# Performance work log

Hardware: AMD Instinct MI355X
Metric: run time of the kernel (lower is better)

The kernel has to match this reference:

```python
import jax, jax.numpy as jnp
import numpy as np


def soft_threshold24(w):
    """2:4 soft-threshold along the last dim: in each contiguous group of 4,
    zero the two smallest magnitudes and shrink the two largest by the
    second-smallest magnitude (sign(w) * relu(|w| - t))."""
    M, N = w.shape
    g = w.reshape(M, N // 4, 4)
    a = jnp.abs(g)
    thr = jnp.sort(a, axis=-1)[..., 1:2]  # 2nd-smallest magnitude per group
    s = jnp.sign(g) * jnp.maximum(a - thr, 0.0)
    return s.reshape(M, N)


def mm_fp16(a, b):
    """fake_fp8_mm: cast operands to fp16, accumulate in fp32."""
    return jnp.matmul(a.astype(jnp.float16), b.astype(jnp.float16),
                      preferred_element_type=jnp.float32)


def setup_inputs() -> dict:
    key = jax.random.key(0)
    k0, k1, k2, k3 = jax.random.split(key, 4)
    B, S, D, R = 4, 2048, 2048, 512
    return {
        "x": jax.random.normal(k0, (B, S, D), jnp.float32),
        "weight_in": jax.random.normal(k1, (D, R), jnp.float32) * 0.02,
        "weight_out": jax.random.normal(k2, (D, R), jnp.float32) * 0.02,
        "bias": jax.random.normal(k3, (D,), jnp.float32) * 0.01,
        "sparse_scale_in": jnp.array(1.0, jnp.float32),
        "sparse_scale_out": jnp.array(1.0, jnp.float32),
    }


def reference(x, weight_in, weight_out, bias, sparse_scale_in, sparse_scale_out):
    B, S, D = x.shape
    # stage 1: x @ sparse24(weight_in) * scale_in  -> [B,S,R]
    win_s = soft_threshold24(weight_in) * sparse_scale_in          # [D, R]
    h = mm_fp16(x.reshape(-1, D), win_s)                            # [B*S, R] fp32
    # stage 2: h @ sparse24(weight_out.T) * scale_out + bias -> [B,S,D]
    wout_s = soft_threshold24(weight_out.T) * sparse_scale_out      # [R, D]
    out = mm_fp16(h, wout_s) + bias                                 # [B*S, D]
    return out.reshape(B, S, D)
```

## Files before the change

kernel.cpp:

```cpp
#include <hip/hip_runtime.h>

typedef _Float16 f16;
typedef _Float16 f16x8 __attribute__((ext_vector_type(8)));
typedef float f32x4 __attribute__((ext_vector_type(4)));

#define BM 128
#define BK 32

__device__ __forceinline__ void g2l16(const f16* g, f16* l) {
    __builtin_amdgcn_global_load_lds(
        (const __attribute__((address_space(1))) void*)g,
        (__attribute__((address_space(3))) void*)l, 16, 0, 0);
}

__device__ __forceinline__ float soft1(float a, float thr, float w, float s) {
    return copysignf(fmaxf(a - thr, 0.0f), w) * s;
}

__device__ __forceinline__ float thr4(float a0, float a1, float a2, float a3) {
    float lo01 = fminf(a0, a1), hi01 = fmaxf(a0, a1);
    float lo23 = fminf(a2, a3), hi23 = fmaxf(a2, a3);
    return fminf(fmaxf(lo01, lo23), fminf(hi01, hi23));
}

__global__ __launch_bounds__(256) void prep_kernel(
    const float* __restrict__ x, f16* __restrict__ xh, int n8,
    const float* __restrict__ Wi, f16* __restrict__ winT, const float* __restrict__ sci,
    const float* __restrict__ Wo, f16* __restrict__ woutT, const float* __restrict__ sco,
    int D, int R, int nCastB, int nSpInB)
{
    int b = blockIdx.x;
    int tid = threadIdx.x;
    if (b < nCastB) {
        int i = b * 256 + tid;
        if (i < n8) {
            float4 a = reinterpret_cast<const float4*>(x)[2 * i];
            float4 c = reinterpret_cast<const float4*>(x)[2 * i + 1];
            f16x8 o = {(f16)a.x, (f16)a.y, (f16)a.z, (f16)a.w,
                       (f16)c.x, (f16)c.y, (f16)c.z, (f16)c.w};
            reinterpret_cast<f16x8*>(xh)[i] = o;
        }
    } else if (b < nCastB + nSpInB) {
        int t = (b - nCastB) * 256 + tid;
        int RG = R >> 2;
        if (t >= RG * D) return;
        int rg = t / D, d = t - rg * D;
        float s = *sci;
        float4 w = *reinterpret_cast<const float4*>(Wi + (size_t)d * R + rg * 4);
        float a0 = fabsf(w.x), a1 = fabsf(w.y), a2 = fabsf(w.z), a3 = fabsf(w.w);
        float thr = thr4(a0, a1, a2, a3);
        size_t base = (size_t)(rg * 4) * D + d;
        winT[base]                 = (f16)soft1(a0, thr, w.x, s);
        winT[base + D]             = (f16)soft1(a1, thr, w.y, s);
        winT[base + 2 * (size_t)D] = (f16)soft1(a2, thr, w.z, s);
        winT[base + 3 * (size_t)D] = (f16)soft1(a3, thr, w.w, s);
    } else {
        int t = (b - nCastB - nSpInB) * 256 + tid;
        if (t >= (D >> 2) * R) return;
        int dg = t / R, r = t - dg * R;
        float s = *sco;
        size_t i0 = (size_t)(dg * 4) * R + r;
        float w0 = Wo[i0], w1 = Wo[i0 + R], w2 = Wo[i0 + 2 * (size_t)R], w3 = Wo[i0 + 3 * (size_t)R];
        float a0 = fabsf(w0), a1 = fabsf(w1), a2 = fabsf(w2), a3 = fabsf(w3);
        float thr = thr4(a0, a1, a2, a3);
        woutT[i0]                 = (f16)soft1(a0, thr, w0, s);
        woutT[i0 + R]             = (f16)soft1(a1, thr, w1, s);
        woutT[i0 + 2 * (size_t)R] = (f16)soft1(a2, thr, w2, s);
        woutT[i0 + 3 * (size_t)R] = (f16)soft1(a3, thr, w3, s);
    }
}

template <int TBN, typename OT, bool BIAS>
__global__ __launch_bounds__(256) void gemm_bt(
    const f16* __restrict__ A, const f16* __restrict__ Bt, OT* __restrict__ C,
    const float* __restrict__ bias, int M, int N, int K)
{
    constexpr int NF = TBN / 32;
    constexpr int HN = TBN / 2;
    __shared__ f16 As[BM * BK];
    __shared__ f16 Bs[TBN * BK];

    const int tid  = threadIdx.x;
    const int lane = tid & 63;
    const int w    = tid >> 6;
    const int wm   = w & 1;
    const int wn   = w >> 1;
    const int l16  = lane & 15;
    const int quad = lane >> 4;
    const int bm = blockIdx.y * BM;
    const int bn = blockIdx.x * TBN;

    const int srow = lane >> 2;
    const int scol = (lane & 3) * 8;
    const f16* gA = A  + (size_t)(bm + w * 32 + srow) * K + scol;
    const f16* gB = Bt + (size_t)(bn + w * (TBN / 4) + srow) * K + scol;
    f16* lA = &As[(w * 32) * BK];
    f16* lB = &Bs[(w * (TBN / 4)) * BK];

    f32x4 acc[4][NF] = {};

    for (int k0 = 0; k0 < K; k0 += BK) {
        g2l16(gA + k0,                  lA);
        g2l16(gA + k0 + 16 * (size_t)K, lA + 16 * BK);
#pragma unroll
        for (int i = 0; i < TBN / 64; ++i)
            g2l16(gB + k0 + i * 16 * (size_t)K, lB + i * 16 * BK);
        __syncthreads();

        f16x8 af[4], bf[NF];
#pragma unroll
        for (int m = 0; m < 4; ++m)
            af[m] = *reinterpret_cast<const f16x8*>(&As[(wm * 64 + m * 16 + l16) * BK + quad * 8]);
#pragma unroll
        for (int n = 0; n < NF; ++n)
            bf[n] = *reinterpret_cast<const f16x8*>(&Bs[(wn * HN + n * 16 + l16) * BK + quad * 8]);
#pragma unroll
        for (int m = 0; m < 4; ++m)
#pragma unroll
            for (int n = 0; n < NF; ++n)
                acc[m][n] = __builtin_amdgcn_mfma_f32_16x16x32_f16(af[m], bf[n], acc[m][n], 0, 0, 0);
        __syncthreads();
    }

#pragma unroll
    for (int m = 0; m < 4; ++m) {
        int row_base = bm + wm * 64 + m * 16 + quad * 4;
#pragma unroll
        for (int n = 0; n < NF; ++n) {
            int col = bn + wn * HN + n * 16 + l16;
            float b = BIAS ? bias[col] : 0.0f;
#pragma unroll
            for (int r = 0; r < 4; ++r) {
                float v = acc[m][n][r];
                size_t idx = (size_t)(row_base + r) * N + col;
                if constexpr (BIAS) C[idx] = (OT)(v + b);
                else                C[idx] = (OT)v;
            }
        }
    }
}

extern "C" void kernel_launch(void* const* d_in, const int* in_sizes, int n_in,
                              void* d_out, int out_size, void* d_ws, size_t ws_size,
                              hipStream_t stream)
{
    const float* x      = (const float*)d_in[0];
    const float* w_in   = (const float*)d_in[1];
    const float* w_out  = (const float*)d_in[2];
    const float* bias   = (const float*)d_in[3];
    const float* sc_in  = (const float*)d_in[4];
    const float* sc_out = (const float*)d_in[5];

    const int D = in_sizes[3];
    const int R = in_sizes[1] / D;
    const int M = in_sizes[0] / D;

    f16* winT  = (f16*)d_ws;
    f16* woutT = winT + (size_t)R * D;
    f16* h     = woutT + (size_t)D * R;
    f16* xh    = h + (size_t)M * R;
    float* out = (float*)d_out;

    const int n8 = M * D / 8;
    const int nCastB  = (n8 + 255) / 256;
    const int nSpInB  = ((R / 4) * D + 255) / 256;
    const int nSpOutB = ((D / 4) * R + 255) / 256;
    prep_kernel<<<nCastB + nSpInB + nSpOutB, 256, 0, stream>>>(
        x, xh, n8, w_in, winT, sc_in, w_out, woutT, sc_out, D, R, nCastB, nSpInB);

    gemm_bt<64, f16, false><<<dim3(R / 64, M / BM), 256, 0, stream>>>(
        xh, winT, h, nullptr, M, R, D);
    gemm_bt<128, float, true><<<dim3(D / 128, M / BM), 256, 0, stream>>>(
        h, woutT, out, bias, M, D, R);
}
```

Measured before the change: 198.8 us.

## Fuse x fp32-to-fp16 cast into GEMM1 loads, shrink tiles, swizzle block order

Drops the separate pass that cast x to fp16. GEMM1 now loads fp32 x tiles straight into LDS and converts them to fp16 when building MFMA fragments, which avoids writing and re-reading a 32MB fp16 copy. Both GEMMs move to 64-row tiles with a 1D grid whose block index is remapped so groups of 8 row-blocks share a column, aiming for more blocks and better L2 reuse. The cost is more LDS traffic per A element in GEMM1 and a smaller MFMA-to-load ratio per block.

```diff
diff --git a/kernel.cpp b/kernel.cpp
--- a/kernel.cpp
+++ b/kernel.cpp
@@ -4,10 +4,9 @@
 typedef _Float16 f16x8 __attribute__((ext_vector_type(8)));
 typedef float f32x4 __attribute__((ext_vector_type(4)));
 
-#define BM 128
 #define BK 32
 
-__device__ __forceinline__ void g2l16(const f16* g, f16* l) {
+__device__ __forceinline__ void g2l16(const void* g, void* l) {
     __builtin_amdgcn_global_load_lds(
         (const __attribute__((address_space(1))) void*)g,
         (__attribute__((address_space(3))) void*)l, 16, 0, 0);
@@ -23,25 +22,22 @@
     return fminf(fmaxf(lo01, lo23), fminf(hi01, hi23));
 }
 
+template <int nCol>
+__device__ __forceinline__ void decode_rc(int bid, int& r, int& c) {
+    int hi = bid >> 3;
+    r = ((hi / nCol) << 3) | (bid & 7);
+    c = hi % nCol;
+}
+
 __global__ __launch_bounds__(256) void prep_kernel(
-    const float* __restrict__ x, f16* __restrict__ xh, int n8,
     const float* __restrict__ Wi, f16* __restrict__ winT, const float* __restrict__ sci,
     const float* __restrict__ Wo, f16* __restrict__ woutT, const float* __restrict__ sco,
-    int D, int R, int nCastB, int nSpInB)
+    int D, int R, int nSpInB)
 {
     int b = blockIdx.x;
     int tid = threadIdx.x;
-    if (b < nCastB) {
-        int i = b * 256 + tid;
-        if (i < n8) {
-            float4 a = reinterpret_cast<const float4*>(x)[2 * i];
-            float4 c = reinterpret_cast<const float4*>(x)[2 * i + 1];
-            f16x8 o = {(f16)a.x, (f16)a.y, (f16)a.z, (f16)a.w,
-                       (f16)c.x, (f16)c.y, (f16)c.z, (f16)c.w};
-            reinterpret_cast<f16x8*>(xh)[i] = o;
-        }
-    } else if (b < nCastB + nSpInB) {
-        int t = (b - nCastB) * 256 + tid;
+    if (b < nSpInB) {
+        int t = b * 256 + tid;
         int RG = R >> 2;
         if (t >= RG * D) return;
         int rg = t / D, d = t - rg * D;
@@ -55,7 +51,7 @@
         winT[base + 2 * (size_t)D] = (f16)soft1(a2, thr, w.z, s);
         winT[base + 3 * (size_t)D] = (f16)soft1(a3, thr, w.w, s);
     } else {
-        int t = (b - nCastB - nSpInB) * 256 + tid;
+        int t = (b - nSpInB) * 256 + tid;
         if (t >= (D >> 2) * R) return;
         int dg = t / R, r = t - dg * R;
         float s = *sco;
@@ -70,15 +66,12 @@
     }
 }
 
-template <int TBN, typename OT, bool BIAS>
-__global__ __launch_bounds__(256) void gemm_bt(
-    const f16* __restrict__ A, const f16* __restrict__ Bt, OT* __restrict__ C,
-    const float* __restrict__ bias, int M, int N, int K)
-{
-    constexpr int NF = TBN / 32;
-    constexpr int HN = TBN / 2;
-    __shared__ f16 As[BM * BK];
-    __shared__ f16 Bs[TBN * BK];
+__global__ __launch_bounds__(256) void gemm1_f32a(
+    const float* __restrict__ A, const f16* __restrict__ Bt, f16* __restrict__ C,
+    int M, int N, int K)
+{
+    __shared__ float Asf[64 * BK];
+    __shared__ f16   Bs[64 * BK];
 
     const int tid  = threadIdx.x;
     const int lane = tid & 63;
@@ -87,55 +80,122 @@
     const int wn   = w >> 1;
     const int l16  = lane & 15;
     const int quad = lane >> 4;
-    const int bm = blockIdx.y * BM;
-    const int bn = blockIdx.x * TBN;
+
+    int rb, cb;
+    decode_rc<8>(blockIdx.x, rb, cb);
+    const int bm = rb * 64;
+    const int bn = cb * 64;
+
+    const int sArow = lane >> 3;
+    const int sAcol = (lane & 7) * 4;
+    const float* gA = A + (size_t)(bm + w * 16 + sArow) * K + sAcol;
+    float* lA = &Asf[(w * 16) * BK];
+    const int sBrow = lane >> 2;
+    const int sBcol = (lane & 3) * 8;
+    const f16* gB = Bt + (size_t)(bn + w * 16 + sBrow) * K + sBcol;
+    f16* lB = &Bs[(w * 16) * BK];
+
+    f32x4 acc[2][2] = {};
+
+    for (int k0 = 0; k0 < K; k0 += BK) {
+        g2l16(gA + k0,                 lA);
+        g2l16(gA + k0 + 8 * (size_t)K, lA + 8 * BK);
+        g2l16(gB + k0,                 lB);
+        __syncthreads();
+
+        f16x8 af[2], bf[2];
+#pragma unroll
+        for (int m = 0; m < 2; ++m) {
+            const float* p = &Asf[(wm * 32 + m * 16 + l16) * BK + quad * 8];
+            float4 u = *reinterpret_cast<const float4*>(p);
+            float4 v = *reinterpret_cast<const float4*>(p + 4);
+            af[m] = f16x8{(f16)u.x, (f16)u.y, (f16)u.z, (f16)u.w,
+                          (f16)v.x, (f16)v.y, (f16)v.z, (f16)v.w};
+        }
+#pragma unroll
+        for (int n = 0; n < 2; ++n)
+            bf[n] = *reinterpret_cast<const f16x8*>(&Bs[(wn * 32 + n * 16 + l16) * BK + quad * 8]);
+#pragma unroll
+        for (int m = 0; m < 2; ++m)
+#pragma unroll
+            for (int n = 0; n < 2; ++n)
+                acc[m][n] = __builtin_amdgcn_mfma_f32_16x16x32_f16(af[m], bf[n], acc[m][n], 0, 0, 0);
+        __syncthreads();
+    }
+
+#pragma unroll
+    for (int m = 0; m < 2; ++m) {
+        int row_base = bm + wm * 32 + m * 16 + quad * 4;
+#pragma unroll
+        for (int n = 0; n < 2; ++n) {
+            int col = bn + wn * 32 + n * 16 + l16;
+#pragma unroll
+            for (int r = 0; r < 4; ++r)
+                C[(size_t)(row_base + r) * N + col] = (f16)acc[m][n][r];
+        }
+    }
+}
+
+__global__ __launch_bounds__(256) void gemm2_bias(
+    const f16* __restrict__ A, const f16* __restrict__ Bt, float* __restrict__ C,
+    const float* __restrict__ bias, int M, int N, int K)
+{
+    __shared__ f16 As[64 * BK];
+    __shared__ f16 Bs[128 * BK];
+
+    const int tid  = threadIdx.x;
+    const int lane = tid & 63;
+    const int w    = tid >> 6;
+    const int wm   = w & 1;
+    const int wn   = w >> 1;
+    const int l16  = lane & 15;
+    const int quad = lane >> 4;
+
+    int rb, cb;
+    decode_rc<16>(blockIdx.x, rb, cb);
+    const int bm = rb * 64;
+    const int bn = cb * 128;
 
     const int srow = lane >> 2;
     const int scol = (lane & 3) * 8;
-    const f16* gA = A  + (size_t)(bm + w * 32 + srow) * K + scol;
-    const f16* gB = Bt + (size_t)(bn + w * (TBN / 4) + srow) * K + scol;
-    f16* lA = &As[(w * 32) * BK];
-    f16* lB = &Bs[(w * (TBN / 4)) * BK];
-
-    f32x4 acc[4][NF] = {};
+    const f16* gA = A  + (size_t)(bm + w * 16 + srow) * K + scol;
+    const f16* gB = Bt + (size_t)(bn + w * 32 + srow) * K + scol;
+    f16* lA = &As[(w * 16) * BK];
+    f16* lB = &Bs[(w * 32) * BK];
+
+    f32x4 acc[2][4] = {};
 
     for (int k0 = 0; k0 < K; k0 += BK) {
         g2l16(gA + k0,                  lA);
-        g2l16(gA + k0 + 16 * (size_t)K, lA + 16 * BK);
-#pragma unroll
-        for (int i = 0; i < TBN / 64; ++i)
-            g2l16(gB + k0 + i * 16 * (size_t)K, lB + i * 16 * BK);
-        __syncthreads();
-
-        f16x8 af[4], bf[NF];
-#pragma unroll
-        for (int m = 0; m < 4; ++m)
-            af[m] = *reinterpret_cast<const f16x8*>(&As[(wm * 64 + m * 16 + l16) * BK + quad * 8]);
-#pragma unroll
-        for (int n = 0; n < NF; ++n)
-            bf[n] = *reinterpret_cast<const f16x8*>(&Bs[(wn * HN + n * 16 + l16) * BK + quad * 8]);
-#pragma unroll
-        for (int m = 0; m < 4; ++m)
-#pragma unroll
-            for (int n = 0; n < NF; ++n)
+        g2l16(gB + k0,                  lB);
+        g2l16(gB + k0 + 16 * (size_t)K, lB + 16 * BK);
+        __syncthreads();
+
+        f16x8 af[2], bf[4];
+#pragma unroll
+        for (int m = 0; m < 2; ++m)
+            af[m] = *reinterpret_cast<const f16x8*>(&As[(wm * 32 + m * 16 + l16) * BK + quad * 8]);
+#pragma unroll
+        for (int n = 0; n < 4; ++n)
+            bf[n] = *reinterpret_cast<const f16x8*>(&Bs[(wn * 64 + n * 16 + l16) * BK + quad * 8]);
+#pragma unroll
+        for (int m = 0; m < 2; ++m)
+#pragma unroll
+            for (int n = 0; n < 4; ++n)
                 acc[m][n] = __builtin_amdgcn_mfma_f32_16x16x32_f16(af[m], bf[n], acc[m][n], 0, 0, 0);
         __syncthreads();
     }
 
 #pragma unroll
-    for (int m = 0; m < 4; ++m) {
-        int row_base = bm + wm * 64 + m * 16 + quad * 4;
-#pragma unroll
-        for (int n = 0; n < NF; ++n) {
-            int col = bn + wn * HN + n * 16 + l16;
-            float b = BIAS ? bias[col] : 0.0f;
-#pragma unroll
-            for (int r = 0; r < 4; ++r) {
-                float v = acc[m][n][r];
-                size_t idx = (size_t)(row_base + r) * N + col;
-                if constexpr (BIAS) C[idx] = (OT)(v + b);
-                else                C[idx] = (OT)v;
-            }
+    for (int m = 0; m < 2; ++m) {
+        int row_base = bm + wm * 32 + m * 16 + quad * 4;
+#pragma unroll
+        for (int n = 0; n < 4; ++n) {
+            int col = bn + wn * 64 + n * 16 + l16;
+            float b = bias[col];
+#pragma unroll
+            for (int r = 0; r < 4; ++r)
+                C[(size_t)(row_base + r) * N + col] = acc[m][n][r] + b;
         }
     }
 }
@@ -158,18 +218,13 @@
     f16* winT  = (f16*)d_ws;
     f16* woutT = winT + (size_t)R * D;
     f16* h     = woutT + (size_t)D * R;
-    f16* xh    = h + (size_t)M * R;
     float* out = (float*)d_out;
 
-    const int n8 = M * D / 8;
-    const int nCastB  = (n8 + 255) / 256;
     const int nSpInB  = ((R / 4) * D + 255) / 256;
     const int nSpOutB = ((D / 4) * R + 255) / 256;
-    prep_kernel<<<nCastB + nSpInB + nSpOutB, 256, 0, stream>>>(
-        x, xh, n8, w_in, winT, sc_in, w_out, woutT, sc_out, D, R, nCastB, nSpInB);
-
-    gemm_bt<64, f16, false><<<dim3(R / 64, M / BM), 256, 0, stream>>>(
-        xh, winT, h, nullptr, M, R, D);
-    gemm_bt<128, float, true><<<dim3(D / 128, M / BM), 256, 0, stream>>>(
-        h, woutT, out, bias, M, D, R);
-}
+    prep_kernel<<<nSpInB + nSpOutB, 256, 0, stream>>>(
+        w_in, winT, sc_in, w_out, woutT, sc_out, D, R, nSpInB);
+
+    gemm1_f32a<<<(M / 64) * (R / 64), 256, 0, stream>>>(x, winT, h, M, R, D);
+    gemm2_bias<<<(M / 64) * (D / 128), 256, 0, stream>>>(h, woutT, out, bias, M, D, R);
+}
```

Result: slower. 326.9 us (+64.4%).
